# Performance work log

Measured on AMD Instinct MI355X. Metric: run time of the kernel, lower is better.

## Reference

```python
import jax, jax.numpy as jnp
import numpy as np

N = 100000      # nodes
E = 1600000     # edges
D_IN, D_H, D_OUT = 256, 64, 47


def setup_inputs() -> dict:
    key = jax.random.key(0)
    k0, k1, k2, k3 = jax.random.split(key, 4)
    x = jax.random.normal(k0, (N, D_IN), dtype=jnp.float32)
    edge_index = jax.random.randint(k1, (2, E), 0, N, dtype=jnp.int64)
    W1 = jax.random.normal(k2, (D_IN, D_H), dtype=jnp.float32) / np.sqrt(D_IN)
    b1 = jnp.zeros((D_H,), dtype=jnp.float32)
    W2 = jax.random.normal(k3, (D_H, D_OUT), dtype=jnp.float32) / np.sqrt(D_H)
    b2 = jnp.zeros((D_OUT,), dtype=jnp.float32)
    return {"x": x, "edge_index": edge_index, "W1": W1, "b1": b1, "W2": W2, "b2": b2}


def _gcn_conv(x, W, b, src, dst, norm):
    # PyG GCNConv: h = x @ W, then scatter_add(norm * h[src] -> dst), + bias
    h = x @ W                                     # [N, out]
    msg = norm[:, None] * h[src]                  # [E+N, out] gather
    out = jax.ops.segment_sum(msg, dst, num_segments=N)  # scatter-add
    return out + b


def reference(x, edge_index, W1, b1, W2, b2):
    # add self-loops with weight 1 (PyG default, edge_weight=None -> ones)
    loop = jnp.arange(N, dtype=edge_index.dtype)
    src = jnp.concatenate([edge_index[0], loop])
    dst = jnp.concatenate([edge_index[1], loop])
    w = jnp.ones((E + N,), dtype=x.dtype)
    # symmetric normalization: deg^-1/2[src] * w * deg^-1/2[dst]
    deg = jax.ops.segment_sum(w, dst, num_segments=N)
    dinv = jnp.where(deg > 0, jax.lax.rsqrt(deg), 0.0)
    norm = dinv[src] * w * dinv[dst]              # [E+N]

    h = _gcn_conv(x, W1, b1, src, dst, norm)
    h = jax.nn.relu(h)
    # F.dropout(training=self.training): eval mode -> identity
    xo = _gcn_conv(h, W2, b2, src, dst, norm)     # [N, D_OUT]
    logits = jax.nn.softmax(xo, axis=1)           # nn.Softmax() -> dim=1 for 2D
    preds = jnp.argmax(logits, axis=1)
    return (logits, preds, xo)
```

## Files before the change

### kernel.cpp

```cpp
#include <hip/hip_runtime.h>
#include <math.h>

#define NN 100000
#define NE 1600000
#define DI 256
#define DH 64
#define DO 47
#define DH3 48
#define NB ((NN + 255) / 256)
#define RSZ8 ((NN + 7) / 8)
#define EPB 2048
#define CPB ((NE + EPB - 1) / EPB)

__global__ __launch_bounds__(256) void k_degree(const int* __restrict__ dst,
                                                int* __restrict__ deg) {
    int r = blockIdx.x & 7;
    int chunk = blockIdx.x >> 3;
    int lo = r * RSZ8, hi = min(lo + RSZ8, NN);
    int base = chunk * EPB + threadIdx.x;
    #pragma unroll
    for (int i = 0; i < EPB / 256; ++i) {
        int e = base + i * 256;
        if (e < NE) {
            int d = dst[e];
            if (d >= lo && d < hi) atomicAdd(&deg[d], 1);
        }
    }
}

__global__ __launch_bounds__(256) void k_part(const int* __restrict__ deg,
                                              int* __restrict__ part) {
    int i = blockIdx.x * 256 + threadIdx.x;
    int v = (i < NN) ? deg[i] : 0;
    for (int off = 32; off; off >>= 1) v += __shfl_xor(v, off);
    __shared__ int s[4];
    if ((threadIdx.x & 63) == 0) s[threadIdx.x >> 6] = v;
    __syncthreads();
    if (threadIdx.x == 0) part[blockIdx.x] = s[0] + s[1] + s[2] + s[3];
}

__global__ __launch_bounds__(512) void k_scanpart(int* __restrict__ part) {
    int t = threadIdx.x, lane = t & 63, wv = t >> 6;
    int v0 = (t < NB) ? part[t] : 0;
    int v = v0;
    for (int off = 1; off < 64; off <<= 1) {
        int u = __shfl_up(v, off);
        if (lane >= off) v += u;
    }
    __shared__ int ws[8];
    if (lane == 63) ws[wv] = v;
    __syncthreads();
    if (t == 0) {
        int run = 0;
        for (int w = 0; w < 8; ++w) { int tmp = ws[w]; ws[w] = run; run += tmp; }
    }
    __syncthreads();
    v += ws[wv];
    if (t < NB) part[t] = v - v0;
}

__global__ __launch_bounds__(256) void k_scan3(const int* __restrict__ deg,
                                               const int* __restrict__ part,
                                               int* __restrict__ rowptr,
                                               int* __restrict__ cursor,
                                               float* __restrict__ dinv) {
    int i = blockIdx.x * 256 + threadIdx.x;
    int lane = threadIdx.x & 63, wv = threadIdx.x >> 6;
    int v0 = (i < NN) ? deg[i] : 0;
    int v = v0;
    for (int off = 1; off < 64; off <<= 1) {
        int u = __shfl_up(v, off);
        if (lane >= off) v += u;
    }
    __shared__ int ws[4], wo[4];
    if (lane == 63) ws[wv] = v;
    __syncthreads();
    if (threadIdx.x == 0) {
        int run = 0;
        for (int w = 0; w < 4; ++w) { int tmp = ws[w]; wo[w] = run; run += tmp; }
    }
    __syncthreads();
    int excl = part[blockIdx.x] + wo[wv] + v - v0;
    if (i < NN) {
        rowptr[i] = excl;
        cursor[i] = excl;
        dinv[i] = rsqrtf((float)(v0 + 1));
    }
}

__global__ __launch_bounds__(256) void k_fillr(const int* __restrict__ src,
                                               const int* __restrict__ dst,
                                               int* __restrict__ cursor,
                                               int* __restrict__ csr_src) {
    int r = blockIdx.x & 7;
    int chunk = blockIdx.x >> 3;
    int lo = r * RSZ8, hi = min(lo + RSZ8, NN);
    int base = chunk * EPB + threadIdx.x;
    #pragma unroll
    for (int i = 0; i < EPB / 256; ++i) {
        int e = base + i * 256;
        if (e < NE) {
            int d = dst[e];
            if (d >= lo && d < hi) {
                int p = atomicAdd(&cursor[d], 1);
                csr_src[p] = src[e];
            }
        }
    }
}

__global__ __launch_bounds__(512) void k_gemm1(const float* __restrict__ x,
                                               const float* __restrict__ W1,
                                               const float* __restrict__ dinv,
                                               float* __restrict__ h1s) {
    __shared__ float xs[2][128 * 33];
    __shared__ float wl[2][32 * 64];
    const int t = threadIdx.x;
    const int lane = t & 63;
    const int wvu = __builtin_amdgcn_readfirstlane(t >> 6);
    const int r0 = blockIdx.x * 128;
    const int sr = t >> 2;
    const int sk = (t & 3) * 8;
    const int wk = t >> 4;
    const int wc = (t & 15) * 4;
    const long xrow = (long)min(r0 + sr, NN - 1) * DI;
    const int rowA = r0 + lane;
    const int rowB = r0 + 64 + lane;

    float accA[8] = {0.f, 0.f, 0.f, 0.f, 0.f, 0.f, 0.f, 0.f};
    float accB[8] = {0.f, 0.f, 0.f, 0.f, 0.f, 0.f, 0.f, 0.f};

    {
        float4 v0 = *(const float4*)(x + xrow + sk);
        float4 v1 = *(const float4*)(x + xrow + sk + 4);
        float* p = &xs[0][sr * 33 + sk];
        p[0] = v0.x; p[1] = v0.y; p[2] = v0.z; p[3] = v0.w;
        p[4] = v1.x; p[5] = v1.y; p[6] = v1.z; p[7] = v1.w;
        float4 w = *(const float4*)(W1 + (size_t)wk * DH + wc);
        float* q = &wl[0][wk * 64 + wc];
        q[0] = w.x; q[1] = w.y; q[2] = w.z; q[3] = w.w;
    }
    __syncthreads();
    for (int c = 0; c < 8; ++c) {
        const int buf = c & 1;
        if (c + 1 < 8) {
            float4 v0 = *(const float4*)(x + xrow + (c + 1) * 32 + sk);
            float4 v1 = *(const float4*)(x + xrow + (c + 1) * 32 + sk + 4);
            float* p = &xs[buf ^ 1][sr * 33 + sk];
            p[0] = v0.x; p[1] = v0.y; p[2] = v0.z; p[3] = v0.w;
            p[4] = v1.x; p[5] = v1.y; p[6] = v1.z; p[7] = v1.w;
            float4 w = *(const float4*)(W1 + (size_t)((c + 1) * 32 + wk) * DH + wc);
            float* q = &wl[buf ^ 1][wk * 64 + wc];
            q[0] = w.x; q[1] = w.y; q[2] = w.z; q[3] = w.w;
        }
        #pragma unroll 4
        for (int kk = 0; kk < 32; ++kk) {
            float xa = xs[buf][lane * 33 + kk];
            float xb = xs[buf][(lane + 64) * 33 + kk];
            const float4* wp = (const float4*)&wl[buf][kk * 64 + wvu * 8];
            float4 wa = wp[0], wb = wp[1];
            accA[0] += wa.x * xa; accA[1] += wa.y * xa;
            accA[2] += wa.z * xa; accA[3] += wa.w * xa;
            accA[4] += wb.x * xa; accA[5] += wb.y * xa;
            accA[6] += wb.z * xa; accA[7] += wb.w * xa;
            accB[0] += wa.x * xb; accB[1] += wa.y * xb;
            accB[2] += wa.z * xb; accB[3] += wa.w * xb;
            accB[4] += wb.x * xb; accB[5] += wb.y * xb;
            accB[6] += wb.z * xb; accB[7] += wb.w * xb;
        }
        __syncthreads();
    }
    if (rowA < NN) {
        float di = dinv[rowA];
        float4 o0 = {di * accA[0], di * accA[1], di * accA[2], di * accA[3]};
        float4 o1 = {di * accA[4], di * accA[5], di * accA[6], di * accA[7]};
        float4* hp = (float4*)(h1s + (long)rowA * DH + wvu * 8);
        hp[0] = o0;
        hp[1] = o1;
    }
    if (rowB < NN) {
        float di = dinv[rowB];
        float4 o0 = {di * accB[0], di * accB[1], di * accB[2], di * accB[3]};
        float4 o1 = {di * accB[4], di * accB[5], di * accB[6], di * accB[7]};
        float4* hp = (float4*)(h1s + (long)rowB * DH + wvu * 8);
        hp[0] = o0;
        hp[1] = o1;
    }
}

__global__ __launch_bounds__(256) void k_agg1(const int* __restrict__ rowptr,
                                              const int* __restrict__ deg,
                                              const int* __restrict__ csr_src,
                                              const float* __restrict__ dinv,
                                              const float* __restrict__ h1s,
                                              const float* __restrict__ b1,
                                              const float* __restrict__ W2,
                                              float* __restrict__ h3s) {
    __shared__ float w2[DH * DO];
    __shared__ float sh[8][DH];
    for (int i = threadIdx.x; i < DH * DO; i += 256) w2[i] = W2[i];
    __syncthreads();
    const int wv = threadIdx.x >> 6, lane = threadIdx.x & 63;
    const int rA = blockIdx.x * 8 + wv * 2;
    const int rB = rA + 1;
    const int begA = rowptr[rA], cntA = deg[rA];
    const int begB = rowptr[rB], cntB = deg[rB];
    float accA = 0.f, accB = 0.f;
    const int tmax = max(cntA, cntB);
    #pragma unroll 2
    for (int j = 0; j < tmax; j += 4) {
        #pragma unroll
        for (int k = 0; k < 4; ++k) {
            int sa = csr_src[min(begA + j + k, NE - 1)];
            int sb = csr_src[min(begB + j + k, NE - 1)];
            float va = h1s[(size_t)sa * DH + lane];
            float vb = h1s[(size_t)sb * DH + lane];
            accA += (j + k < cntA) ? va : 0.f;
            accB += (j + k < cntB) ? vb : 0.f;
        }
    }
    const float diA = dinv[rA], diB = dinv[rB];
    float vA = diA * (accA + h1s[(size_t)rA * DH + lane]) + b1[lane];
    float vB = diB * (accB + h1s[(size_t)rB * DH + lane]) + b1[lane];
    sh[wv * 2 + 0][lane] = fmaxf(vA, 0.f);
    sh[wv * 2 + 1][lane] = fmaxf(vB, 0.f);
    __syncthreads();
    if (lane < DO) {
        float oA = 0.f, oB = 0.f;
        #pragma unroll 8
        for (int k = 0; k < DH; ++k) {
            float w = w2[k * DO + lane];
            oA += sh[wv * 2 + 0][k] * w;
            oB += sh[wv * 2 + 1][k] * w;
        }
        h3s[(size_t)rA * DH3 + lane] = diA * oA;
        h3s[(size_t)rB * DH3 + lane] = diB * oB;
    }
}

__global__ __launch_bounds__(256) void k_agg2(const int* __restrict__ rowptr,
                                              const int* __restrict__ deg,
                                              const int* __restrict__ csr_src,
                                              const float* __restrict__ dinv,
                                              const float* __restrict__ h3s,
                                              const float* __restrict__ b2,
                                              float* __restrict__ logits,
                                              float* __restrict__ preds,
                                              float* __restrict__ xo) {
    const int wv = threadIdx.x >> 6, lane = threadIdx.x & 63;
    const int rA = blockIdx.x * 8 + wv * 2;
    const int rB = rA + 1;
    const int begA = rowptr[rA], cntA = deg[rA];
    const int begB = rowptr[rB], cntB = deg[rB];
    const bool act = lane < DO;
    const int lx = act ? lane : 0;
    float accA = 0.f, accB = 0.f;
    const int tmax = max(cntA, cntB);
    #pragma unroll 2
    for (int j = 0; j < tmax; j += 4) {
        #pragma unroll
        for (int k = 0; k < 4; ++k) {
            int sa = csr_src[min(begA + j + k, NE - 1)];
            int sb = csr_src[min(begB + j + k, NE - 1)];
            float va = h3s[(size_t)sa * DH3 + lx];
            float vb = h3s[(size_t)sb * DH3 + lx];
            accA += (j + k < cntA) ? va : 0.f;
            accB += (j + k < cntB) ? vb : 0.f;
        }
    }
    const float diA = dinv[rA], diB = dinv[rB];
    float valA = -INFINITY, valB = -INFINITY;
    if (act) {
        valA = diA * (accA + h3s[(size_t)rA * DH3 + lane]) + b2[lane];
        valB = diB * (accB + h3s[(size_t)rB * DH3 + lane]) + b2[lane];
        xo[(size_t)rA * DO + lane] = valA;
        xo[(size_t)rB * DO + lane] = valB;
    }
    float mA = valA, mB = valB;
    for (int off = 32; off; off >>= 1) {
        mA = fmaxf(mA, __shfl_xor(mA, off));
        mB = fmaxf(mB, __shfl_xor(mB, off));
    }
    int idxA = (act && valA == mA) ? lane : (1 << 30);
    int idxB = (act && valB == mB) ? lane : (1 << 30);
    for (int off = 32; off; off >>= 1) {
        idxA = min(idxA, __shfl_xor(idxA, off));
        idxB = min(idxB, __shfl_xor(idxB, off));
    }
    float evA = act ? expf(valA - mA) : 0.f;
    float evB = act ? expf(valB - mB) : 0.f;
    float sA = evA, sB = evB;
    for (int off = 32; off; off >>= 1) {
        sA += __shfl_xor(sA, off);
        sB += __shfl_xor(sB, off);
    }
    if (act) {
        logits[(size_t)rA * DO + lane] = evA / sA;
        logits[(size_t)rB * DO + lane] = evB / sB;
    }
    if (lane == 0) {
        preds[rA] = (float)idxA;
        preds[rB] = (float)idxB;
    }
}

extern "C" void kernel_launch(void* const* d_in, const int* in_sizes, int n_in,
                              void* d_out, int out_size, void* d_ws, size_t ws_size,
                              hipStream_t stream) {
    const float* x  = (const float*)d_in[0];
    const int*   ei = (const int*)d_in[1];
    const float* W1 = (const float*)d_in[2];
    const float* b1 = (const float*)d_in[3];
    const float* W2 = (const float*)d_in[4];
    const float* b2 = (const float*)d_in[5];
    const int* src = ei;
    const int* dst = ei + NE;

    float* out    = (float*)d_out;
    float* logits = out;
    float* preds  = out + (size_t)NN * DO;
    float* xo     = preds + NN;

    char* wsb = (char*)d_ws;
    int*   deg     = (int*)wsb;                         wsb += (size_t)NN * 4;
    float* dinv    = (float*)wsb;                       wsb += (size_t)NN * 4;
    int*   rowptr  = (int*)wsb;                         wsb += (size_t)NN * 4;
    int*   cursor  = (int*)wsb;                         wsb += (size_t)NN * 4;
    int*   part    = (int*)wsb;                         wsb += (size_t)512 * 4;
    int*   csr_src = (int*)wsb;                         wsb += (size_t)NE * 4;
    float* h1s     = (float*)wsb;                       wsb += (size_t)NN * DH * 4;
    float* h3s     = (float*)wsb;                       wsb += (size_t)NN * DH3 * 4;

    hipMemsetAsync(deg, 0, NN * sizeof(int), stream);

    k_degree<<<8 * CPB, 256, 0, stream>>>(dst, deg);
    k_part<<<NB, 256, 0, stream>>>(deg, part);
    k_scanpart<<<1, 512, 0, stream>>>(part);
    k_scan3<<<NB, 256, 0, stream>>>(deg, part, rowptr, cursor, dinv);
    k_fillr<<<8 * CPB, 256, 0, stream>>>(src, dst, cursor, csr_src);
    k_gemm1<<<(NN + 127) / 128, 512, 0, stream>>>(x, W1, dinv, h1s);
    k_agg1<<<NN / 8, 256, 0, stream>>>(rowptr, deg, csr_src, dinv, h1s, b1, W2, h3s);
    k_agg2<<<NN / 8, 256, 0, stream>>>(rowptr, deg, csr_src, dinv, h3s, b2, logits, preds, xo);
}
```

Baseline: 350.1 us.

## Vectorize GCN aggregation gathers with float4 loads across four edges per wave

Both aggregation kernels now split each wave into 4 edge groups of 16 lanes, each lane loading a float4 of the neighbor feature row. That processes 4 edges per iteration per row instead of one scalar per lane, and reduces the partial sums with cross-lane shuffles. There is an unmasked main loop over the shared minimum degree plus a masked tail, and the softmax/argmax epilogue is reworked to handle 4 values per lane. The aim is fewer, wider memory instructions and more memory parallelism in the gathers. In exchange it adds shuffle reductions and idles lanes in the epilogue.

```diff
diff --git a/kernel.cpp b/kernel.cpp
--- a/kernel.cpp
+++ b/kernel.cpp
@@ -201,29 +201,66 @@
     for (int i = threadIdx.x; i < DH * DO; i += 256) w2[i] = W2[i];
     __syncthreads();
     const int wv = threadIdx.x >> 6, lane = threadIdx.x & 63;
-    const int rA = blockIdx.x * 8 + wv * 2;
-    const int rB = rA + 1;
+    const int c = lane & 15, e = lane >> 4;
+    const unsigned c4 = (unsigned)(c * 4);
+    const int rA = blockIdx.x * 8 + wv * 2, rB = rA + 1;
     const int begA = rowptr[rA], cntA = deg[rA];
     const int begB = rowptr[rB], cntB = deg[rB];
-    float accA = 0.f, accB = 0.f;
-    const int tmax = max(cntA, cntB);
-    #pragma unroll 2
-    for (int j = 0; j < tmax; j += 4) {
-        #pragma unroll
-        for (int k = 0; k < 4; ++k) {
-            int sa = csr_src[min(begA + j + k, NE - 1)];
-            int sb = csr_src[min(begB + j + k, NE - 1)];
-            float va = h1s[(size_t)sa * DH + lane];
-            float vb = h1s[(size_t)sb * DH + lane];
-            accA += (j + k < cntA) ? va : 0.f;
-            accB += (j + k < cntB) ? vb : 0.f;
-        }
-    }
+    float aAx = 0.f, aAy = 0.f, aAz = 0.f, aAw = 0.f;
+    float aBx = 0.f, aBy = 0.f, aBz = 0.f, aBw = 0.f;
+    const int cmin = min(cntA, cntB), tmax = max(cntA, cntB);
+    int j = 0;
+    for (; j + 7 < cmin; j += 8) {
+        unsigned sa0 = (unsigned)csr_src[begA + j + e];
+        unsigned sb0 = (unsigned)csr_src[begB + j + e];
+        unsigned sa1 = (unsigned)csr_src[begA + j + 4 + e];
+        unsigned sb1 = (unsigned)csr_src[begB + j + 4 + e];
+        float4 va0 = *(const float4*)(h1s + sa0 * 64u + c4);
+        float4 vb0 = *(const float4*)(h1s + sb0 * 64u + c4);
+        float4 va1 = *(const float4*)(h1s + sa1 * 64u + c4);
+        float4 vb1 = *(const float4*)(h1s + sb1 * 64u + c4);
+        aAx += va0.x + va1.x; aAy += va0.y + va1.y;
+        aAz += va0.z + va1.z; aAw += va0.w + va1.w;
+        aBx += vb0.x + vb1.x; aBy += vb0.y + vb1.y;
+        aBz += vb0.z + vb1.z; aBw += vb0.w + vb1.w;
+    }
+    for (; j < tmax; j += 4) {
+        unsigned sa = (unsigned)csr_src[min(begA + j + e, NE - 1)];
+        unsigned sb = (unsigned)csr_src[min(begB + j + e, NE - 1)];
+        float4 va = *(const float4*)(h1s + sa * 64u + c4);
+        float4 vb = *(const float4*)(h1s + sb * 64u + c4);
+        float mA = (j + e < cntA) ? 1.f : 0.f;
+        float mB = (j + e < cntB) ? 1.f : 0.f;
+        aAx = fmaf(mA, va.x, aAx); aAy = fmaf(mA, va.y, aAy);
+        aAz = fmaf(mA, va.z, aAz); aAw = fmaf(mA, va.w, aAw);
+        aBx = fmaf(mB, vb.x, aBx); aBy = fmaf(mB, vb.y, aBy);
+        aBz = fmaf(mB, vb.z, aBz); aBw = fmaf(mB, vb.w, aBw);
+    }
+    aAx += __shfl_xor(aAx, 16); aAx += __shfl_xor(aAx, 32);
+    aAy += __shfl_xor(aAy, 16); aAy += __shfl_xor(aAy, 32);
+    aAz += __shfl_xor(aAz, 16); aAz += __shfl_xor(aAz, 32);
+    aAw += __shfl_xor(aAw, 16); aAw += __shfl_xor(aAw, 32);
+    aBx += __shfl_xor(aBx, 16); aBx += __shfl_xor(aBx, 32);
+    aBy += __shfl_xor(aBy, 16); aBy += __shfl_xor(aBy, 32);
+    aBz += __shfl_xor(aBz, 16); aBz += __shfl_xor(aBz, 32);
+    aBw += __shfl_xor(aBw, 16); aBw += __shfl_xor(aBw, 32);
     const float diA = dinv[rA], diB = dinv[rB];
-    float vA = diA * (accA + h1s[(size_t)rA * DH + lane]) + b1[lane];
-    float vB = diB * (accB + h1s[(size_t)rB * DH + lane]) + b1[lane];
-    sh[wv * 2 + 0][lane] = fmaxf(vA, 0.f);
-    sh[wv * 2 + 1][lane] = fmaxf(vB, 0.f);
+    if (lane < 16) {
+        float4 sA = *(const float4*)(h1s + (unsigned)rA * 64u + c4);
+        float4 sB = *(const float4*)(h1s + (unsigned)rB * 64u + c4);
+        float4 bb = *(const float4*)(b1 + c4);
+        float4 oA, oB;
+        oA.x = fmaxf(diA * (aAx + sA.x) + bb.x, 0.f);
+        oA.y = fmaxf(diA * (aAy + sA.y) + bb.y, 0.f);
+        oA.z = fmaxf(diA * (aAz + sA.z) + bb.z, 0.f);
+        oA.w = fmaxf(diA * (aAw + sA.w) + bb.w, 0.f);
+        oB.x = fmaxf(diB * (aBx + sB.x) + bb.x, 0.f);
+        oB.y = fmaxf(diB * (aBy + sB.y) + bb.y, 0.f);
+        oB.z = fmaxf(diB * (aBz + sB.z) + bb.z, 0.f);
+        oB.w = fmaxf(diB * (aBw + sB.w) + bb.w, 0.f);
+        *(float4*)&sh[wv * 2 + 0][c4] = oA;
+        *(float4*)&sh[wv * 2 + 1][c4] = oB;
+    }
     __syncthreads();
     if (lane < DO) {
         float oA = 0.f, oB = 0.f;
@@ -233,8 +270,8 @@
             oA += sh[wv * 2 + 0][k] * w;
             oB += sh[wv * 2 + 1][k] * w;
         }
-        h3s[(size_t)rA * DH3 + lane] = diA * oA;
-        h3s[(size_t)rB * DH3 + lane] = diB * oB;
+        h3s[(unsigned)rA * DH3 + lane] = diA * oA;
+        h3s[(unsigned)rB * DH3 + lane] = diB * oB;
     }
 }
 
@@ -248,59 +285,97 @@
                                               float* __restrict__ preds,
                                               float* __restrict__ xo) {
     const int wv = threadIdx.x >> 6, lane = threadIdx.x & 63;
-    const int rA = blockIdx.x * 8 + wv * 2;
-    const int rB = rA + 1;
+    const int c = lane & 15, e = lane >> 4;
+    const unsigned cc4 = (unsigned)(((c < 12) ? c : 0) * 4);
+    const int rA = blockIdx.x * 8 + wv * 2, rB = rA + 1;
     const int begA = rowptr[rA], cntA = deg[rA];
     const int begB = rowptr[rB], cntB = deg[rB];
-    const bool act = lane < DO;
-    const int lx = act ? lane : 0;
-    float accA = 0.f, accB = 0.f;
-    const int tmax = max(cntA, cntB);
-    #pragma unroll 2
-    for (int j = 0; j < tmax; j += 4) {
-        #pragma unroll
-        for (int k = 0; k < 4; ++k) {
-            int sa = csr_src[min(begA + j + k, NE - 1)];
-            int sb = csr_src[min(begB + j + k, NE - 1)];
-            float va = h3s[(size_t)sa * DH3 + lx];
-            float vb = h3s[(size_t)sb * DH3 + lx];
-            accA += (j + k < cntA) ? va : 0.f;
-            accB += (j + k < cntB) ? vb : 0.f;
-        }
-    }
+    float aAx = 0.f, aAy = 0.f, aAz = 0.f, aAw = 0.f;
+    float aBx = 0.f, aBy = 0.f, aBz = 0.f, aBw = 0.f;
+    const int cmin = min(cntA, cntB), tmax = max(cntA, cntB);
+    int j = 0;
+    for (; j + 7 < cmin; j += 8) {
+        unsigned sa0 = (unsigned)csr_src[begA + j + e];
+        unsigned sb0 = (unsigned)csr_src[begB + j + e];
+        unsigned sa1 = (unsigned)csr_src[begA + j + 4 + e];
+        unsigned sb1 = (unsigned)csr_src[begB + j + 4 + e];
+        float4 va0 = *(const float4*)(h3s + sa0 * 48u + cc4);
+        float4 vb0 = *(const float4*)(h3s + sb0 * 48u + cc4);
+        float4 va1 = *(const float4*)(h3s + sa1 * 48u + cc4);
+        float4 vb1 = *(const float4*)(h3s + sb1 * 48u + cc4);
+        aAx += va0.x + va1.x; aAy += va0.y + va1.y;
+        aAz += va0.z + va1.z; aAw += va0.w + va1.w;
+        aBx += vb0.x + vb1.x; aBy += vb0.y + vb1.y;
+        aBz += vb0.z + vb1.z; aBw += vb0.w + vb1.w;
+    }
+    for (; j < tmax; j += 4) {
+        unsigned sa = (unsigned)csr_src[min(begA + j + e, NE - 1)];
+        unsigned sb = (unsigned)csr_src[min(begB + j + e, NE - 1)];
+        float4 va = *(const float4*)(h3s + sa * 48u + cc4);
+        float4 vb = *(const float4*)(h3s + sb * 48u + cc4);
+        float mA = (j + e < cntA) ? 1.f : 0.f;
+        float mB = (j + e < cntB) ? 1.f : 0.f;
+        aAx = fmaf(mA, va.x, aAx); aAy = fmaf(mA, va.y, aAy);
+        aAz = fmaf(mA, va.z, aAz); aAw = fmaf(mA, va.w, aAw);
+        aBx = fmaf(mB, vb.x, aBx); aBy = fmaf(mB, vb.y, aBy);
+        aBz = fmaf(mB, vb.z, aBz); aBw = fmaf(mB, vb.w, aBw);
+    }
+    aAx += __shfl_xor(aAx, 16); aAx += __shfl_xor(aAx, 32);
+    aAy += __shfl_xor(aAy, 16); aAy += __shfl_xor(aAy, 32);
+    aAz += __shfl_xor(aAz, 16); aAz += __shfl_xor(aAz, 32);
+    aAw += __shfl_xor(aAw, 16); aAw += __shfl_xor(aAw, 32);
+    aBx += __shfl_xor(aBx, 16); aBx += __shfl_xor(aBx, 32);
+    aBy += __shfl_xor(aBy, 16); aBy += __shfl_xor(aBy, 32);
+    aBz += __shfl_xor(aBz, 16); aBz += __shfl_xor(aBz, 32);
+    aBw += __shfl_xor(aBw, 16); aBw += __shfl_xor(aBw, 32);
     const float diA = dinv[rA], diB = dinv[rB];
-    float valA = -INFINITY, valB = -INFINITY;
-    if (act) {
-        valA = diA * (accA + h3s[(size_t)rA * DH3 + lane]) + b2[lane];
-        valB = diB * (accB + h3s[(size_t)rB * DH3 + lane]) + b2[lane];
-        xo[(size_t)rA * DO + lane] = valA;
-        xo[(size_t)rB * DO + lane] = valB;
-    }
-    float mA = valA, mB = valB;
-    for (int off = 32; off; off >>= 1) {
-        mA = fmaxf(mA, __shfl_xor(mA, off));
-        mB = fmaxf(mB, __shfl_xor(mB, off));
-    }
-    int idxA = (act && valA == mA) ? lane : (1 << 30);
-    int idxB = (act && valB == mB) ? lane : (1 << 30);
-    for (int off = 32; off; off >>= 1) {
-        idxA = min(idxA, __shfl_xor(idxA, off));
-        idxB = min(idxB, __shfl_xor(idxB, off));
-    }
-    float evA = act ? expf(valA - mA) : 0.f;
-    float evB = act ? expf(valB - mB) : 0.f;
-    float sA = evA, sB = evB;
-    for (int off = 32; off; off >>= 1) {
-        sA += __shfl_xor(sA, off);
-        sB += __shfl_xor(sB, off);
-    }
-    if (act) {
-        logits[(size_t)rA * DO + lane] = evA / sA;
-        logits[(size_t)rB * DO + lane] = evB / sB;
-    }
-    if (lane == 0) {
-        preds[rA] = (float)idxA;
-        preds[rB] = (float)idxB;
+    const bool lv = (lane < 16) && (c < 12);
+    float b0 = 0.f, bq1 = 0.f, bq2 = 0.f, bq3 = 0.f;
+    if (lv) {
+        b0 = b2[c * 4 + 0]; bq1 = b2[c * 4 + 1]; bq2 = b2[c * 4 + 2];
+        bq3 = (c < 11) ? b2[c * 4 + 3] : 0.f;
+    }
+    #pragma unroll
+    for (int rr = 0; rr < 2; ++rr) {
+        const int row = rr ? rB : rA;
+        const float di = rr ? diB : diA;
+        float ax = rr ? aBx : aAx, ay = rr ? aBy : aAy;
+        float az = rr ? aBz : aAz, aw = rr ? aBw : aAw;
+        float vx = -INFINITY, vy = -INFINITY, vz = -INFINITY, vw = -INFINITY;
+        if (lv) {
+            float4 sf = *(const float4*)(h3s + (unsigned)row * 48u + cc4);
+            vx = di * (ax + sf.x) + b0;
+            vy = di * (ay + sf.y) + bq1;
+            vz = di * (az + sf.z) + bq2;
+            vw = (c < 11) ? (di * (aw + sf.w) + bq3) : -INFINITY;
+            float* xp = xo + (size_t)row * DO + c * 4;
+            xp[0] = vx; xp[1] = vy; xp[2] = vz;
+            if (c < 11) xp[3] = vw;
+        }
+        float lm = fmaxf(fmaxf(vx, vy), fmaxf(vz, vw));
+        float gm = lm;
+        for (int off = 32; off; off >>= 1) gm = fmaxf(gm, __shfl_xor(gm, off));
+        int cand = 1 << 30;
+        if (lv) {
+            if (vx == gm) cand = c * 4 + 0;
+            else if (vy == gm) cand = c * 4 + 1;
+            else if (vz == gm) cand = c * 4 + 2;
+            else if (c < 11 && vw == gm) cand = c * 4 + 3;
+        }
+        for (int off = 32; off; off >>= 1) cand = min(cand, __shfl_xor(cand, off));
+        float e0 = 0.f, e1 = 0.f, e2 = 0.f, e3 = 0.f;
+        if (lv) {
+            e0 = expf(vx - gm); e1 = expf(vy - gm); e2 = expf(vz - gm);
+            e3 = (c < 11) ? expf(vw - gm) : 0.f;
+        }
+        float gs = e0 + e1 + e2 + e3;
+        for (int off = 32; off; off >>= 1) gs += __shfl_xor(gs, off);
+        if (lv) {
+            float* lp = logits + (size_t)row * DO + c * 4;
+            lp[0] = e0 / gs; lp[1] = e1 / gs; lp[2] = e2 / gs;
+            if (c < 11) lp[3] = e3 / gs;
+        }
+        if (lane == 0) preds[row] = (float)cand;
     }
 }
 
```

Result: slower. 371.5 us (+6.1%).
